# Performance work log

Measured on AMD Instinct MI355X. Metric: run time of the kernel, lower is better.

## Reference

```python
import jax, jax.numpy as jnp
import numpy as np

B, S, D, H = 1, 2048, 2048, 16
HD = D // H
I = 8192
EPS = 1e-5
NEG = -1e9


def setup_inputs() -> dict:
    key = jax.random.key(0)
    ks = jax.random.split(key, 9)
    x = jax.random.normal(ks[0], (B, S, D), jnp.float32)
    # causal additive mask
    causal = jnp.triu(jnp.full((S, S), NEG, jnp.float32), k=1)[None, None]
    # RoPE tables (duplicated-half convention matching rotate_half)
    inv_freq = 1.0 / (10000.0 ** (np.arange(0, HD, 2, dtype=np.float32) / HD))
    t = np.arange(S, dtype=np.float32)
    freqs = np.outer(t, inv_freq)  # [S, HD/2]
    emb = np.concatenate([freqs, freqs], axis=-1)  # [S, HD]
    freqs_cos = jnp.asarray(np.cos(emb))[None, None]  # [1,1,S,HD]
    freqs_sin = jnp.asarray(np.sin(emb))[None, None]
    scale = 0.02
    return {
        "x": x,
        "attention_mask": causal,
        "freqs_cos": freqs_cos,
        "freqs_sin": freqs_sin,
        "wq": jax.random.normal(ks[1], (D, D), jnp.float32) * scale,
        "wk": jax.random.normal(ks[2], (D, D), jnp.float32) * scale,
        "wv": jax.random.normal(ks[3], (D, D), jnp.float32) * scale,
        "wo": jax.random.normal(ks[4], (D, D), jnp.float32) * scale,
        "w1": jax.random.normal(ks[5], (D, I), jnp.float32) * scale,
        "w2": jax.random.normal(ks[6], (I, D), jnp.float32) * scale,
        "w3": jax.random.normal(ks[7], (D, I), jnp.float32) * scale,
        "attn_norm_w": jnp.ones((D,), jnp.float32),
        "ffn_norm_w": jnp.ones((D,), jnp.float32),
    }


def rms_norm(x, w):
    xf = x.astype(jnp.float32)
    n = xf * jax.lax.rsqrt(jnp.mean(xf * xf, axis=-1, keepdims=True) + EPS)
    return w * n.astype(x.dtype)


def rotate_half(x):
    x1, x2 = jnp.split(x, 2, axis=-1)
    return jnp.concatenate([-x2, x1], axis=-1)


def reference(x, attention_mask, freqs_cos, freqs_sin, wq, wk, wv, wo, w1, w2, w3, attn_norm_w, ffn_norm_w):
    nx = rms_norm(x, attn_norm_w)
    # project and split heads -> [B, H, S, HD]
    def heads(y, w):
        return (y @ w).reshape(B, S, H, HD).transpose(0, 2, 1, 3)
    q = heads(nx, wq)
    k = heads(nx, wk)
    v = heads(nx, wv)
    q = q * freqs_cos + rotate_half(q) * freqs_sin
    k = k * freqs_cos + rotate_half(k) * freqs_sin
    scores = jnp.einsum("bhqd,bhkd->bhqk", q, k) / jnp.sqrt(jnp.float32(HD))
    scores = scores + attention_mask
    attn = jax.nn.softmax(scores, axis=-1)
    out = jnp.einsum("bhqk,bhkd->bhqd", attn, v)
    out = out.transpose(0, 2, 1, 3).reshape(B, S, D) @ wo
    x = x + out
    nx = rms_norm(x, ffn_norm_w)
    ff = (jax.nn.silu(nx @ w1) * (nx @ w3)) @ w2
    return x + ff
```

## Files before the change

kernel.cpp:

```cpp
#include <hip/hip_runtime.h>

typedef unsigned short u16;
typedef __bf16 bf16_t;
typedef bf16_t bf16x8 __attribute__((ext_vector_type(8)));
typedef float f32x4 __attribute__((ext_vector_type(4)));

#define D_MODEL 2048
#define SEQ     2048
#define NHEAD   16
#define HDIM    128
#define IDIM    8192
#define QKV_LD  6144

__device__ __forceinline__ u16 f2bf(float f) {
    unsigned u = __float_as_uint(f);
    u += 0x7fffu + ((u >> 16) & 1u);
    return (u16)(u >> 16);
}
__device__ __forceinline__ float bf2f(u16 u) {
    return __uint_as_float(((unsigned)u) << 16);
}
__device__ __forceinline__ void gload16(const void* g, void* l) {
    __builtin_amdgcn_global_load_lds(
        (const __attribute__((address_space(1))) unsigned int*)g,
        (__attribute__((address_space(3))) unsigned int*)l, 16, 0, 0);
}
#define MFMA16(a, b, c) __builtin_amdgcn_mfma_f32_16x16x32_bf16((a), (b), (c), 0, 0, 0)

__global__ __launch_bounds__(256) void rmsnorm_kernel(
    const float* __restrict__ x, const float* __restrict__ w, u16* __restrict__ out)
{
    int row = blockIdx.x, t = threadIdx.x;
    const float4* xr = (const float4*)(x + (size_t)row * D_MODEL);
    float4 a = xr[t * 2], b = xr[t * 2 + 1];
    float ss = a.x*a.x + a.y*a.y + a.z*a.z + a.w*a.w
             + b.x*b.x + b.y*b.y + b.z*b.z + b.w*b.w;
#pragma unroll
    for (int off = 32; off > 0; off >>= 1) ss += __shfl_down(ss, off, 64);
    __shared__ float red[4];
    __shared__ float sinv;
    if ((t & 63) == 0) red[t >> 6] = ss;
    __syncthreads();
    if (t == 0) sinv = rsqrtf((red[0] + red[1] + red[2] + red[3]) * (1.0f / D_MODEL) + 1e-5f);
    __syncthreads();
    float inv = sinv;
    const float4* w4 = (const float4*)w;
    float4 wa = w4[t * 2], wb = w4[t * 2 + 1];
    u16* o = out + (size_t)row * D_MODEL + t * 8;
    o[0] = f2bf(a.x * inv * wa.x); o[1] = f2bf(a.y * inv * wa.y);
    o[2] = f2bf(a.z * inv * wa.z); o[3] = f2bf(a.w * inv * wa.w);
    o[4] = f2bf(b.x * inv * wb.x); o[5] = f2bf(b.y * inv * wb.y);
    o[6] = f2bf(b.z * inv * wb.z); o[7] = f2bf(b.w * inv * wb.w);
}

__global__ __launch_bounds__(256) void tcvt_kernel(
    const float* __restrict__ src, u16* __restrict__ dst, int R, int C)
{
    __shared__ float tile[32][33];
    int tx = threadIdx.x & 31, ty = threadIdx.x >> 5;
    int c = blockIdx.x * 32 + tx;
    int rb = blockIdx.y * 32;
#pragma unroll
    for (int i = 0; i < 32; i += 8)
        tile[ty + i][tx] = src[(size_t)(rb + ty + i) * C + c];
    __syncthreads();
    int dr = blockIdx.x * 32 + ty;
    int dc = rb + tx;
#pragma unroll
    for (int i = 0; i < 32; i += 8)
        dst[(size_t)(dr + i) * R + dc] = f2bf(tile[tx][ty + i]);
}

__global__ __launch_bounds__(256) void tbf16_kernel(
    const u16* __restrict__ src, u16* __restrict__ dst, int R, int C, int ld)
{
    __shared__ u16 tile[32][34];
    int tx = threadIdx.x & 31, ty = threadIdx.x >> 5;
    int c = blockIdx.x * 32 + tx;
    int rb = blockIdx.y * 32;
#pragma unroll
    for (int i = 0; i < 32; i += 8)
        tile[ty + i][tx] = src[(size_t)(rb + ty + i) * ld + c];
    __syncthreads();
    int dr = blockIdx.x * 32 + ty;
    int dc = rb + tx;
#pragma unroll
    for (int i = 0; i < 32; i += 8)
        dst[(size_t)(dr + i) * R + dc] = tile[tx][ty + i];
}

__global__ __launch_bounds__(256) void rope_kernel(
    u16* __restrict__ qkv, const float* __restrict__ fc, const float* __restrict__ fs)
{
    int s = blockIdx.x, t = threadIdx.x;
    const float* cr = fc + (size_t)s * HDIM;
    const float* sr = fs + (size_t)s * HDIM;
#pragma unroll
    for (int p = 0; p < 4; p++) {
        int pi = p * 256 + t;
        int h = pi >> 6, d = pi & 63;
        size_t base = (size_t)s * QKV_LD + h * HDIM + d;
        float c1 = cr[d], s1 = sr[d], c2 = cr[d + 64], s2 = sr[d + 64];
        float q1 = bf2f(qkv[base]), q2 = bf2f(qkv[base + 64]);
        qkv[base]      = f2bf(q1 * c1 - q2 * s1);
        qkv[base + 64] = f2bf(q2 * c2 + q1 * s2);
        size_t kb = base + 2048;
        float k1 = bf2f(qkv[kb]), k2 = bf2f(qkv[kb + 64]);
        qkv[kb]      = f2bf(k1 * c1 - k2 * s1);
        qkv[kb + 64] = f2bf(k2 * c2 + k1 * s2);
    }
}

template <int BM, int EPI>
__global__ __launch_bounds__(256, 3) void gemm_bt(
    const u16* __restrict__ A, const u16* __restrict__ Bt,
    const float* __restrict__ res, const u16* __restrict__ gate,
    float* __restrict__ outf, u16* __restrict__ outb,
    int M, int N, int K, int lda, int ldb)
{
    constexpr int WC = (BM == 128) ? 2 : 4;
    constexpr int MI = 4;
    constexpr int NJ = (BM == 128) ? 4 : 2;
    constexpr int LA = BM / 64;
    __shared__ __align__(16) u16 lA[BM * 32];
    __shared__ __align__(16) u16 lB[128 * 32];
    int t = threadIdx.x;
    int wave = t >> 6, lane = t & 63, quad = lane >> 4, l16 = lane & 15;
    int wr = wave / WC, wc = wave % WC;
    int m0 = blockIdx.y * BM, n0 = blockIdx.x * 128;
    int mb = wr * (MI * 16), nb = wc * (NJ * 16);
    int koff = blockIdx.z * K;

    f32x4 acc[MI][NJ];
    const f32x4 fzero = {0.f, 0.f, 0.f, 0.f};
#pragma unroll
    for (int i = 0; i < MI; i++)
#pragma unroll
        for (int j = 0; j < NJ; j++) acc[i][j] = fzero;

    const u16* gA[LA]; u16* lAp[LA];
#pragma unroll
    for (int l = 0; l < LA; l++) {
        int row = l * 64 + (t >> 2);
        int gch = (t & 3) ^ ((row >> 1) & 3);
        gA[l] = A + (size_t)(m0 + row) * lda + koff + gch * 8;
        lAp[l] = &lA[(l * 256 + t) * 8];
    }
    const u16* gB[2]; u16* lBp[2];
#pragma unroll
    for (int l = 0; l < 2; l++) {
        int row = l * 64 + (t >> 2);
        int gch = (t & 3) ^ ((row >> 1) & 3);
        gB[l] = Bt + (size_t)(n0 + row) * ldb + koff + gch * 8;
        lBp[l] = &lB[(l * 256 + t) * 8];
    }
    int fslot = (quad ^ ((l16 >> 1) & 3)) * 8;

    for (int k0 = 0; k0 < K; k0 += 32) {
#pragma unroll
        for (int l = 0; l < LA; l++) gload16(gA[l] + k0, lAp[l]);
        gload16(gB[0] + k0, lBp[0]);
        gload16(gB[1] + k0, lBp[1]);
        asm volatile("s_waitcnt vmcnt(0)" ::: "memory");
        __syncthreads();
        bf16x8 af[MI], bfv[NJ];
#pragma unroll
        for (int i = 0; i < MI; i++)
            af[i] = *(const bf16x8*)&lA[(mb + i * 16 + l16) * 32 + fslot];
#pragma unroll
        for (int j = 0; j < NJ; j++)
            bfv[j] = *(const bf16x8*)&lB[(nb + j * 16 + l16) * 32 + fslot];
#pragma unroll
        for (int i = 0; i < MI; i++)
#pragma unroll
            for (int j = 0; j < NJ; j++)
                acc[i][j] = MFMA16(af[i], bfv[j], acc[i][j]);
        __syncthreads();
    }

    float* po = (EPI == 3) ? outf + (size_t)blockIdx.z * M * N : outf;
#pragma unroll
    for (int i = 0; i < MI; i++)
#pragma unroll
        for (int j = 0; j < NJ; j++)
#pragma unroll
            for (int r = 0; r < 4; r++) {
                int m = m0 + mb + i * 16 + quad * 4 + r;
                int n = n0 + nb + j * 16 + l16;
                size_t idx = (size_t)m * N + n;
                float v = acc[i][j][r];
                if (EPI == 0) {
                    outb[idx] = f2bf(v);
                } else if (EPI == 1) {
                    outf[idx] = res[idx] + v;
                } else if (EPI == 2) {
                    float g = bf2f(gate[idx]);
                    outb[idx] = f2bf(g / (1.f + __expf(-g)) * v);
                } else {
                    po[idx] = v;
                }
            }
}

__global__ __launch_bounds__(256) void reduce4_kernel(
    const float* __restrict__ x1, const float* __restrict__ part, float* __restrict__ out)
{
    size_t i = (size_t)blockIdx.x * 256 + threadIdx.x;
    float4 a = ((const float4*)x1)[i];
#pragma unroll
    for (int z = 0; z < 4; z++) {
        float4 pv = ((const float4*)(part + (size_t)z * SEQ * D_MODEL))[i];
        a.x += pv.x; a.y += pv.y; a.z += pv.z; a.w += pv.w;
    }
    ((float4*)out)[i] = a;
}

__global__ __launch_bounds__(256, 1) void attn_kernel(
    const u16* __restrict__ q, const u16* __restrict__ k,
    const u16* __restrict__ vt, u16* __restrict__ ctx)
{
    __shared__ __align__(16) u16 sQ[128 * 128];
    __shared__ __align__(16) u16 sK[128 * 128];
    __shared__ __align__(16) u16 sV[128 * 128];
    __shared__ float sRed[2][128];
    __shared__ float sM[128];
    __shared__ float sL[128];

    int t = threadIdx.x;
    int wave = t >> 6, lane = t & 63, quad = lane >> 4, l16 = lane & 15;
    int wr = wave >> 1, wc = wave & 1;
    int h = blockIdx.y, qt = blockIdx.x;
    int q0 = qt * 128;
    int srow = t >> 4, schunk = t & 15;

#pragma unroll
    for (int p = 0; p < 8; p++) {
        int r = p * 16 + srow;
        int gc = schunk ^ (r & 7);
        gload16(q + (size_t)(q0 + r) * QKV_LD + h * HDIM + gc * 8, &sQ[p * 2048 + t * 8]);
    }
    if (t < 128) { sM[t] = -3e38f; sL[t] = 0.f; }
    const f32x4 fzero = {0.f, 0.f, 0.f, 0.f};
    f32x4 o[4][4];
#pragma unroll
    for (int i = 0; i < 4; i++)
#pragma unroll
        for (int j = 0; j < 4; j++) o[i][j] = fzero;
    asm volatile("s_waitcnt vmcnt(0)" ::: "memory");
    __syncthreads();

    const float scale = 0.08838834764831845f;
    int fsw = l16 & 7;

    for (int kt = 0; kt <= qt; kt++) {
        int k0 = kt * 128;
#pragma unroll
        for (int p = 0; p < 8; p++) {
            int r = p * 16 + srow;
            int gc = schunk ^ (r & 7);
            gload16(k + (size_t)(k0 + r) * QKV_LD + h * HDIM + gc * 8, &sK[p * 2048 + t * 8]);
            gload16(vt + (size_t)(h * HDIM + r) * SEQ + k0 + gc * 8, &sV[p * 2048 + t * 8]);
        }
        asm volatile("s_waitcnt vmcnt(0)" ::: "memory");
        __syncthreads();

        f32x4 sc[4][4];
#pragma unroll
        for (int i = 0; i < 4; i++)
#pragma unroll
            for (int j = 0; j < 4; j++) sc[i][j] = fzero;
#pragma unroll
        for (int kk = 0; kk < 4; kk++) {
            int cs = ((kk * 4 + quad) ^ fsw) * 8;
            bf16x8 af[4], bfv[4];
#pragma unroll
            for (int i = 0; i < 4; i++)
                af[i] = *(const bf16x8*)&sQ[(wr * 64 + i * 16 + l16) * 128 + cs];
#pragma unroll
            for (int j = 0; j < 4; j++)
                bfv[j] = *(const bf16x8*)&sK[(wc * 64 + j * 16 + l16) * 128 + cs];
#pragma unroll
            for (int i = 0; i < 4; i++)
#pragma unroll
                for (int j = 0; j < 4; j++)
                    sc[i][j] = MFMA16(af[i], bfv[j], sc[i][j]);
        }

        float rmax[4][4];
#pragma unroll
        for (int i = 0; i < 4; i++)
#pragma unroll
            for (int r = 0; r < 4; r++) {
                int qrow = q0 + wr * 64 + i * 16 + quad * 4 + r;
                float mx = -3e38f;
#pragma unroll
                for (int j = 0; j < 4; j++) {
                    int kcol = k0 + wc * 64 + j * 16 + l16;
                    float v = sc[i][j][r] * scale;
                    v = (kcol <= qrow) ? v : -3e38f;
                    sc[i][j][r] = v;
                    mx = fmaxf(mx, v);
                }
#pragma unroll
                for (int dlt = 1; dlt < 16; dlt <<= 1)
                    mx = fmaxf(mx, __shfl_xor(mx, dlt, 64));
                rmax[i][r] = mx;
            }
        if (l16 == 0) {
#pragma unroll
            for (int i = 0; i < 4; i++)
#pragma unroll
                for (int r = 0; r < 4; r++)
                    sRed[wc][wr * 64 + i * 16 + quad * 4 + r] = rmax[i][r];
        }
        __syncthreads();

        float alpha[4][4], rsum[4][4], mnv[4][4];
#pragma unroll
        for (int i = 0; i < 4; i++)
#pragma unroll
            for (int r = 0; r < 4; r++) {
                int row = wr * 64 + i * 16 + quad * 4 + r;
                float tm = fmaxf(rmax[i][r], sRed[1 - wc][row]);
                float mo = sM[row];
                float mn = fmaxf(mo, tm);
                mnv[i][r] = mn;
                alpha[i][r] = __expf(mo - mn);
                float s = 0.f;
#pragma unroll
                for (int j = 0; j < 4; j++) {
                    float pv = __expf(sc[i][j][r] - mn);
                    sc[i][j][r] = pv;
                    s += pv;
                }
#pragma unroll
                for (int dlt = 1; dlt < 16; dlt <<= 1)
                    s += __shfl_xor(s, dlt, 64);
                rsum[i][r] = s;
            }
        __syncthreads();
        if (l16 == 0) {
#pragma unroll
            for (int i = 0; i < 4; i++)
#pragma unroll
                for (int r = 0; r < 4; r++)
                    sRed[wc][wr * 64 + i * 16 + quad * 4 + r] = rsum[i][r];
        }
#pragma unroll
        for (int i = 0; i < 4; i++)
#pragma unroll
            for (int j = 0; j < 4; j++)
#pragma unroll
                for (int r = 0; r < 4; r++) {
                    int row = wr * 64 + i * 16 + quad * 4 + r;
                    int col = wc * 64 + j * 16 + l16;
                    sK[(col >> 3) * 1024 + row * 8 + (col & 7)] = f2bf(sc[i][j][r]);
                }
#pragma unroll
        for (int i = 0; i < 4; i++)
#pragma unroll
            for (int j = 0; j < 4; j++)
#pragma unroll
                for (int r = 0; r < 4; r++) o[i][j][r] *= alpha[i][r];
        __syncthreads();
        if (wc == 0 && l16 == 0) {
#pragma unroll
            for (int i = 0; i < 4; i++)
#pragma unroll
                for (int r = 0; r < 4; r++) {
                    int row = wr * 64 + i * 16 + quad * 4 + r;
                    float tot = rsum[i][r] + sRed[1][row];
                    sM[row] = mnv[i][r];
                    sL[row] = alpha[i][r] * sL[row] + tot;
                }
        }
#pragma unroll
        for (int kk = 0; kk < 4; kk++) {
            int cs = ((kk * 4 + quad) ^ fsw) * 8;
            bf16x8 af[4], bfv[4];
#pragma unroll
            for (int i = 0; i < 4; i++)
                af[i] = *(const bf16x8*)&sK[(kk * 4 + quad) * 1024 + (wr * 64 + i * 16 + l16) * 8];
#pragma unroll
            for (int j = 0; j < 4; j++)
                bfv[j] = *(const bf16x8*)&sV[(wc * 64 + j * 16 + l16) * 128 + cs];
#pragma unroll
            for (int i = 0; i < 4; i++)
#pragma unroll
                for (int j = 0; j < 4; j++)
                    o[i][j] = MFMA16(af[i], bfv[j], o[i][j]);
        }
        __syncthreads();
    }

#pragma unroll
    for (int i = 0; i < 4; i++)
#pragma unroll
        for (int r = 0; r < 4; r++) {
            int row = wr * 64 + i * 16 + quad * 4 + r;
            float inv = 1.f / sL[row];
#pragma unroll
            for (int j = 0; j < 4; j++) {
                int n = h * HDIM + wc * 64 + j * 16 + l16;
                ctx[(size_t)(q0 + row) * D_MODEL + n] = f2bf(o[i][j][r] * inv);
            }
        }
}

extern "C" void kernel_launch(void* const* d_in, const int* in_sizes, int n_in,
                              void* d_out, int out_size, void* d_ws, size_t ws_size,
                              hipStream_t stream)
{
    const float* x    = (const float*)d_in[0];
    const float* fcos = (const float*)d_in[2];
    const float* fsin = (const float*)d_in[3];
    const float* wq   = (const float*)d_in[4];
    const float* wk   = (const float*)d_in[5];
    const float* wv   = (const float*)d_in[6];
    const float* wo   = (const float*)d_in[7];
    const float* w1   = (const float*)d_in[8];
    const float* w2   = (const float*)d_in[9];
    const float* w3   = (const float*)d_in[10];
    const float* anw  = (const float*)d_in[11];
    const float* fnw  = (const float*)d_in[12];
    float* out = (float*)d_out;

    const size_t MB = 1024 * 1024;
    char* base = (char*)d_ws;
    u16*   qkvT = (u16*)  (base + 0);
    u16*   woT  = (u16*)  (base + 24 * MB);
    u16*   w1T  = (u16*)  (base + 32 * MB);
    u16*   w3T  = (u16*)  (base + 64 * MB);
    u16*   w2T  = (u16*)  (base + 96 * MB);
    u16*   nx   = (u16*)  (base + 128 * MB);
    u16*   qkv  = (u16*)  (base + 136 * MB);
    u16*   vtb  = (u16*)  (base + 160 * MB);
    u16*   ctxb = (u16*)  (base + 168 * MB);
    float* x1   = (float*)(base + 176 * MB);
    u16*   nx2  = (u16*)  (base + 192 * MB);
    u16*   h1b  = (u16*)  (base + 200 * MB);
    u16*   hb   = (u16*)  (base + 232 * MB);
    float* part = (float*)(base + 0);

    dim3 blk(256);

    rmsnorm_kernel<<<SEQ, blk, 0, stream>>>(x, anw, nx);
    tcvt_kernel<<<dim3(64, 64),  blk, 0, stream>>>(wq, qkvT,                       D_MODEL, D_MODEL);
    tcvt_kernel<<<dim3(64, 64),  blk, 0, stream>>>(wk, qkvT + 2048 * 2048,         D_MODEL, D_MODEL);
    tcvt_kernel<<<dim3(64, 64),  blk, 0, stream>>>(wv, qkvT + (size_t)4096 * 2048, D_MODEL, D_MODEL);
    tcvt_kernel<<<dim3(64, 64),  blk, 0, stream>>>(wo, woT, D_MODEL, D_MODEL);
    tcvt_kernel<<<dim3(256, 64), blk, 0, stream>>>(w1, w1T, D_MODEL, IDIM);
    tcvt_kernel<<<dim3(256, 64), blk, 0, stream>>>(w3, w3T, D_MODEL, IDIM);
    tcvt_kernel<<<dim3(64, 256), blk, 0, stream>>>(w2, w2T, IDIM, D_MODEL);

    gemm_bt<128, 0><<<dim3(48, 16), blk, 0, stream>>>(
        nx, qkvT, nullptr, nullptr, nullptr, qkv, SEQ, QKV_LD, D_MODEL, D_MODEL, D_MODEL);

    rope_kernel<<<SEQ, blk, 0, stream>>>(qkv, fcos, fsin);
    tbf16_kernel<<<dim3(64, 64), blk, 0, stream>>>(qkv + 4096, vtb, SEQ, D_MODEL, QKV_LD);

    attn_kernel<<<dim3(16, 16), blk, 0, stream>>>(qkv, qkv + 2048, vtb, ctxb);

    gemm_bt<64, 1><<<dim3(16, 32), blk, 0, stream>>>(
        ctxb, woT, x, nullptr, x1, nullptr, SEQ, D_MODEL, D_MODEL, D_MODEL, D_MODEL);

    rmsnorm_kernel<<<SEQ, blk, 0, stream>>>(x1, fnw, nx2);

    gemm_bt<128, 0><<<dim3(64, 16), blk, 0, stream>>>(
        nx2, w1T, nullptr, nullptr, nullptr, h1b, SEQ, IDIM, D_MODEL, D_MODEL, D_MODEL);
    gemm_bt<128, 2><<<dim3(64, 16), blk, 0, stream>>>(
        nx2, w3T, nullptr, h1b, nullptr, hb, SEQ, IDIM, D_MODEL, D_MODEL, D_MODEL);

    gemm_bt<128, 3><<<dim3(16, 16, 4), blk, 0, stream>>>(
        hb, w2T, nullptr, nullptr, part, nullptr, SEQ, D_MODEL, 2048, IDIM, IDIM);
    reduce4_kernel<<<dim3(4096), blk, 0, stream>>>(x1, part, out);
}
```

Before: 851.9 us.

## Restructure attention to row-per-wave softmax with Q in registers and K prefetch

Result: faster. 788.3 us (-7.5%).

```diff
diff --git a/kernel.cpp b/kernel.cpp
--- a/kernel.cpp
+++ b/kernel.cpp
@@ -219,16 +219,12 @@
     const u16* __restrict__ q, const u16* __restrict__ k,
     const u16* __restrict__ vt, u16* __restrict__ ctx)
 {
-    __shared__ __align__(16) u16 sQ[128 * 128];
-    __shared__ __align__(16) u16 sK[128 * 128];
+    __shared__ __align__(16) u16 sK[2][128 * 128];
     __shared__ __align__(16) u16 sV[128 * 128];
-    __shared__ float sRed[2][128];
-    __shared__ float sM[128];
-    __shared__ float sL[128];
+    __shared__ __align__(16) u16 sP[4][16 * 32 * 8];
 
     int t = threadIdx.x;
     int wave = t >> 6, lane = t & 63, quad = lane >> 4, l16 = lane & 15;
-    int wr = wave >> 1, wc = wave & 1;
     int h = blockIdx.y, qt = blockIdx.x;
     int q0 = qt * 128;
     int srow = t >> 4, schunk = t & 15;
@@ -237,171 +233,183 @@
     for (int p = 0; p < 8; p++) {
         int r = p * 16 + srow;
         int gc = schunk ^ (r & 7);
-        gload16(q + (size_t)(q0 + r) * QKV_LD + h * HDIM + gc * 8, &sQ[p * 2048 + t * 8]);
-    }
-    if (t < 128) { sM[t] = -3e38f; sL[t] = 0.f; }
+        gload16(q + (size_t)(q0 + r) * QKV_LD + h * HDIM + gc * 8, &sK[1][p * 2048 + t * 8]);
+    }
+#pragma unroll
+    for (int p = 0; p < 8; p++) {
+        int r = p * 16 + srow;
+        int gc = schunk ^ (r & 7);
+        gload16(k + (size_t)r * QKV_LD + h * HDIM + gc * 8, &sK[0][p * 2048 + t * 8]);
+    }
+    asm volatile("s_waitcnt vmcnt(0)" ::: "memory");
+    __builtin_amdgcn_s_barrier();
+    __builtin_amdgcn_sched_barrier(0);
+
+    bf16x8 qa[2][4];
+#pragma unroll
+    for (int i = 0; i < 2; i++) {
+        int row = wave * 32 + i * 16 + l16;
+#pragma unroll
+        for (int kk = 0; kk < 4; kk++)
+            qa[i][kk] = *(const bf16x8*)&sK[1][row * 128 + (((kk * 4 + quad) ^ (row & 7)) * 8)];
+    }
+    asm volatile("s_waitcnt lgkmcnt(0)" ::: "memory");
+    __builtin_amdgcn_sched_barrier(0);
+    __builtin_amdgcn_s_barrier();
+    __builtin_amdgcn_sched_barrier(0);
+
+    const float scale = 0.08838834764831845f;
+    float m_r[2][4], l_r[2][4];
+#pragma unroll
+    for (int i = 0; i < 2; i++)
+#pragma unroll
+        for (int r = 0; r < 4; r++) { m_r[i][r] = -3e38f; l_r[i][r] = 0.f; }
     const f32x4 fzero = {0.f, 0.f, 0.f, 0.f};
-    f32x4 o[4][4];
-#pragma unroll
-    for (int i = 0; i < 4; i++)
-#pragma unroll
-        for (int j = 0; j < 4; j++) o[i][j] = fzero;
-    asm volatile("s_waitcnt vmcnt(0)" ::: "memory");
-    __syncthreads();
-
-    const float scale = 0.08838834764831845f;
-    int fsw = l16 & 7;
+    f32x4 o[2][8];
+#pragma unroll
+    for (int i = 0; i < 2; i++)
+#pragma unroll
+        for (int j = 0; j < 8; j++) o[i][j] = fzero;
+    u16* sPw = sP[wave];
 
     for (int kt = 0; kt <= qt; kt++) {
+        int c = kt & 1;
         int k0 = kt * 128;
+
 #pragma unroll
         for (int p = 0; p < 8; p++) {
             int r = p * 16 + srow;
             int gc = schunk ^ (r & 7);
-            gload16(k + (size_t)(k0 + r) * QKV_LD + h * HDIM + gc * 8, &sK[p * 2048 + t * 8]);
             gload16(vt + (size_t)(h * HDIM + r) * SEQ + k0 + gc * 8, &sV[p * 2048 + t * 8]);
         }
-        asm volatile("s_waitcnt vmcnt(0)" ::: "memory");
-        __syncthreads();
-
-        f32x4 sc[4][4];
-#pragma unroll
-        for (int i = 0; i < 4; i++)
-#pragma unroll
-            for (int j = 0; j < 4; j++) sc[i][j] = fzero;
+        if (kt < qt) {
+            int k1 = k0 + 128;
+#pragma unroll
+            for (int p = 0; p < 8; p++) {
+                int r = p * 16 + srow;
+                int gc = schunk ^ (r & 7);
+                gload16(k + (size_t)(k1 + r) * QKV_LD + h * HDIM + gc * 8,
+                        &sK[1 - c][p * 2048 + t * 8]);
+            }
+            asm volatile("s_waitcnt vmcnt(16)" ::: "memory");
+        } else {
+            asm volatile("s_waitcnt vmcnt(8)" ::: "memory");
+        }
+        __builtin_amdgcn_sched_barrier(0);
+        __builtin_amdgcn_s_barrier();
+        __builtin_amdgcn_sched_barrier(0);
+
+        f32x4 sc[2][8];
+#pragma unroll
+        for (int i = 0; i < 2; i++)
+#pragma unroll
+            for (int j = 0; j < 8; j++) sc[i][j] = fzero;
+        const u16* sKc = sK[c];
 #pragma unroll
         for (int kk = 0; kk < 4; kk++) {
-            int cs = ((kk * 4 + quad) ^ fsw) * 8;
-            bf16x8 af[4], bfv[4];
-#pragma unroll
-            for (int i = 0; i < 4; i++)
-                af[i] = *(const bf16x8*)&sQ[(wr * 64 + i * 16 + l16) * 128 + cs];
-#pragma unroll
-            for (int j = 0; j < 4; j++)
-                bfv[j] = *(const bf16x8*)&sK[(wc * 64 + j * 16 + l16) * 128 + cs];
-#pragma unroll
-            for (int i = 0; i < 4; i++)
-#pragma unroll
-                for (int j = 0; j < 4; j++)
-                    sc[i][j] = MFMA16(af[i], bfv[j], sc[i][j]);
-        }
-
-        float rmax[4][4];
-#pragma unroll
-        for (int i = 0; i < 4; i++)
+            bf16x8 kf[8];
+#pragma unroll
+            for (int j = 0; j < 8; j++)
+                kf[j] = *(const bf16x8*)&sKc[(j * 16 + l16) * 128 +
+                                             (((kk * 4 + quad) ^ (l16 & 7)) * 8)];
+#pragma unroll
+            for (int i = 0; i < 2; i++)
+#pragma unroll
+                for (int j = 0; j < 8; j++)
+                    sc[i][j] = MFMA16(qa[i][kk], kf[j], sc[i][j]);
+        }
+
+#pragma unroll
+        for (int i = 0; i < 2; i++)
+#pragma unroll
+            for (int j = 0; j < 8; j++) sc[i][j] = sc[i][j] * scale;
+        if (kt == qt) {
+#pragma unroll
+            for (int i = 0; i < 2; i++)
+#pragma unroll
+                for (int j = 0; j < 8; j++) {
+                    int col = j * 16 + l16;
+#pragma unroll
+                    for (int r = 0; r < 4; r++) {
+                        int row = wave * 32 + i * 16 + quad * 4 + r;
+                        if (col > row) sc[i][j][r] = -3e38f;
+                    }
+                }
+        }
+
+#pragma unroll
+        for (int i = 0; i < 2; i++)
 #pragma unroll
             for (int r = 0; r < 4; r++) {
-                int qrow = q0 + wr * 64 + i * 16 + quad * 4 + r;
-                float mx = -3e38f;
-#pragma unroll
-                for (int j = 0; j < 4; j++) {
-                    int kcol = k0 + wc * 64 + j * 16 + l16;
-                    float v = sc[i][j][r] * scale;
-                    v = (kcol <= qrow) ? v : -3e38f;
-                    sc[i][j][r] = v;
-                    mx = fmaxf(mx, v);
-                }
-#pragma unroll
-                for (int dlt = 1; dlt < 16; dlt <<= 1)
-                    mx = fmaxf(mx, __shfl_xor(mx, dlt, 64));
-                rmax[i][r] = mx;
-            }
-        if (l16 == 0) {
-#pragma unroll
-            for (int i = 0; i < 4; i++)
-#pragma unroll
-                for (int r = 0; r < 4; r++)
-                    sRed[wc][wr * 64 + i * 16 + quad * 4 + r] = rmax[i][r];
-        }
-        __syncthreads();
-
-        float alpha[4][4], rsum[4][4], mnv[4][4];
-#pragma unroll
-        for (int i = 0; i < 4; i++)
-#pragma unroll
-            for (int r = 0; r < 4; r++) {
-                int row = wr * 64 + i * 16 + quad * 4 + r;
-                float tm = fmaxf(rmax[i][r], sRed[1 - wc][row]);
-                float mo = sM[row];
-                float mn = fmaxf(mo, tm);
-                mnv[i][r] = mn;
-                alpha[i][r] = __expf(mo - mn);
+                float mx = sc[i][0][r];
+#pragma unroll
+                for (int j = 1; j < 8; j++) mx = fmaxf(mx, sc[i][j][r]);
+#pragma unroll
+                for (int d = 1; d < 16; d <<= 1) mx = fmaxf(mx, __shfl_xor(mx, d, 64));
+                float mo = m_r[i][r];
+                float mn = fmaxf(mo, mx);
+                float al = __expf(mo - mn);
+                m_r[i][r] = mn;
                 float s = 0.f;
 #pragma unroll
-                for (int j = 0; j < 4; j++) {
+                for (int j = 0; j < 8; j++) {
                     float pv = __expf(sc[i][j][r] - mn);
                     sc[i][j][r] = pv;
                     s += pv;
                 }
 #pragma unroll
-                for (int dlt = 1; dlt < 16; dlt <<= 1)
-                    s += __shfl_xor(s, dlt, 64);
-                rsum[i][r] = s;
+                for (int d = 1; d < 16; d <<= 1) s += __shfl_xor(s, d, 64);
+                l_r[i][r] = al * l_r[i][r] + s;
+#pragma unroll
+                for (int j = 0; j < 8; j++) o[i][j][r] *= al;
+                int rl = i * 16 + quad * 4 + r;
+#pragma unroll
+                for (int j = 0; j < 8; j++) {
+                    int col = j * 16 + l16;
+                    sPw[(col >> 3) * 256 + rl * 8 + (col & 7)] = f2bf(sc[i][j][r]);
+                }
             }
-        __syncthreads();
-        if (l16 == 0) {
-#pragma unroll
-            for (int i = 0; i < 4; i++)
-#pragma unroll
-                for (int r = 0; r < 4; r++)
-                    sRed[wc][wr * 64 + i * 16 + quad * 4 + r] = rsum[i][r];
-        }
-#pragma unroll
-        for (int i = 0; i < 4; i++)
-#pragma unroll
-            for (int j = 0; j < 4; j++)
-#pragma unroll
-                for (int r = 0; r < 4; r++) {
-                    int row = wr * 64 + i * 16 + quad * 4 + r;
-                    int col = wc * 64 + j * 16 + l16;
-                    sK[(col >> 3) * 1024 + row * 8 + (col & 7)] = f2bf(sc[i][j][r]);
-                }
-#pragma unroll
-        for (int i = 0; i < 4; i++)
-#pragma unroll
-            for (int j = 0; j < 4; j++)
-#pragma unroll
-                for (int r = 0; r < 4; r++) o[i][j][r] *= alpha[i][r];
-        __syncthreads();
-        if (wc == 0 && l16 == 0) {
-#pragma unroll
-            for (int i = 0; i < 4; i++)
-#pragma unroll
-                for (int r = 0; r < 4; r++) {
-                    int row = wr * 64 + i * 16 + quad * 4 + r;
-                    float tot = rsum[i][r] + sRed[1][row];
-                    sM[row] = mnv[i][r];
-                    sL[row] = alpha[i][r] * sL[row] + tot;
-                }
-        }
+
+        if (kt < qt) {
+            asm volatile("s_waitcnt vmcnt(8) lgkmcnt(0)" ::: "memory");
+        } else {
+            asm volatile("s_waitcnt vmcnt(0) lgkmcnt(0)" ::: "memory");
+        }
+        __builtin_amdgcn_sched_barrier(0);
+        __builtin_amdgcn_s_barrier();
+        __builtin_amdgcn_sched_barrier(0);
+
 #pragma unroll
         for (int kk = 0; kk < 4; kk++) {
-            int cs = ((kk * 4 + quad) ^ fsw) * 8;
-            bf16x8 af[4], bfv[4];
-#pragma unroll
-            for (int i = 0; i < 4; i++)
-                af[i] = *(const bf16x8*)&sK[(kk * 4 + quad) * 1024 + (wr * 64 + i * 16 + l16) * 8];
-#pragma unroll
-            for (int j = 0; j < 4; j++)
-                bfv[j] = *(const bf16x8*)&sV[(wc * 64 + j * 16 + l16) * 128 + cs];
-#pragma unroll
-            for (int i = 0; i < 4; i++)
-#pragma unroll
-                for (int j = 0; j < 4; j++)
-                    o[i][j] = MFMA16(af[i], bfv[j], o[i][j]);
-        }
-        __syncthreads();
-    }
-
-#pragma unroll
-    for (int i = 0; i < 4; i++)
+            bf16x8 pa[2], vf[8];
+#pragma unroll
+            for (int i = 0; i < 2; i++)
+                pa[i] = *(const bf16x8*)&sPw[(kk * 4 + quad) * 256 + (i * 16 + l16) * 8];
+#pragma unroll
+            for (int j = 0; j < 8; j++)
+                vf[j] = *(const bf16x8*)&sV[(j * 16 + l16) * 128 +
+                                            (((kk * 4 + quad) ^ (l16 & 7)) * 8)];
+#pragma unroll
+            for (int i = 0; i < 2; i++)
+#pragma unroll
+                for (int j = 0; j < 8; j++)
+                    o[i][j] = MFMA16(pa[i], vf[j], o[i][j]);
+        }
+        asm volatile("s_waitcnt lgkmcnt(0)" ::: "memory");
+        __builtin_amdgcn_sched_barrier(0);
+        __builtin_amdgcn_s_barrier();
+        __builtin_amdgcn_sched_barrier(0);
+    }
+
+#pragma unroll
+    for (int i = 0; i < 2; i++)
 #pragma unroll
         for (int r = 0; r < 4; r++) {
-            int row = wr * 64 + i * 16 + quad * 4 + r;
-            float inv = 1.f / sL[row];
-#pragma unroll
-            for (int j = 0; j < 4; j++) {
-                int n = h * HDIM + wc * 64 + j * 16 + l16;
+            int row = wave * 32 + i * 16 + quad * 4 + r;
+            float inv = 1.f / l_r[i][r];
+#pragma unroll
+            for (int j = 0; j < 8; j++) {
+                int n = h * HDIM + j * 16 + l16;
                 ctx[(size_t)(q0 + row) * D_MODEL + n] = f2bf(o[i][j][r] * inv);
             }
         }
```
